# Optimization experiments

Measured on AMD Instinct MI355X. Metric: run time of the kernel, lower is better.

Reference implementation:

```python
import jax, jax.numpy as jnp
import numpy as np

# Mamba2 dims (from source: d_model=2048, d_state=64, d_conv=4, expand=2; defaults headdim=64, ngroups=1)
D_MODEL = 2048
D_STATE = 64
D_CONV = 4
EXPAND = 2
HEADDIM = 64
D_INNER = EXPAND * D_MODEL            # 4096
NHEADS = D_INNER // HEADDIM           # 64
NGROUPS = 1
CONV_DIM = D_INNER + 2 * NGROUPS * D_STATE   # 4224
D_IN_PROJ = 2 * D_INNER + 2 * NGROUPS * D_STATE + NHEADS  # 8384
N_CLASSES = 4
EPS = 1e-5


def setup_inputs() -> dict:
    key = jax.random.key(0)
    ks = jax.random.split(key, 10)
    b, l = 4, 2048
    x = jax.random.normal(ks[0], (b, l, D_MODEL), dtype=jnp.float32)
    in_proj_w = jax.random.normal(ks[1], (D_IN_PROJ, D_MODEL), dtype=jnp.float32) * 0.02
    conv_w = jax.random.normal(ks[2], (CONV_DIM, D_CONV), dtype=jnp.float32) * 0.2
    conv_b = jnp.zeros((CONV_DIM,), dtype=jnp.float32)
    # dt_bias s.t. softplus(dt_bias) in [0.001, 0.1]
    dt = jax.random.uniform(ks[3], (NHEADS,), minval=0.001, maxval=0.1)
    dt_bias = jnp.log(jnp.expm1(dt)).astype(jnp.float32)
    # A in [1, 16] per head
    A_log = jnp.log(jax.random.uniform(ks[4], (NHEADS,), minval=1.0, maxval=16.0)).astype(jnp.float32)
    D = jnp.ones((NHEADS,), dtype=jnp.float32)
    norm_w = jnp.ones((D_INNER,), dtype=jnp.float32)
    out_proj_w = jax.random.normal(ks[5], (D_MODEL, D_INNER), dtype=jnp.float32) * 0.02
    cls_w = jax.random.normal(ks[6], (N_CLASSES, D_MODEL), dtype=jnp.float32) * 0.02
    cls_b = jnp.zeros((N_CLASSES,), dtype=jnp.float32)
    return {"x": x, "in_proj_w": in_proj_w, "conv_w": conv_w, "conv_b": conv_b,
            "dt_bias": dt_bias, "A_log": A_log, "D": D, "norm_w": norm_w,
            "out_proj_w": out_proj_w, "cls_w": cls_w, "cls_b": cls_b}


def _mamba2_forward(x, in_proj_w, conv_w, conv_b, dt_bias, A_log, D, norm_w, out_proj_w):
    b, l, _ = x.shape
    zxbcdt = jnp.einsum('bld,ed->ble', x, in_proj_w)  # (b,l,8384)
    z = zxbcdt[..., :D_INNER]
    xBC = zxbcdt[..., D_INNER:D_INNER + CONV_DIM]
    dt_raw = zxbcdt[..., D_INNER + CONV_DIM:]         # (b,l,nheads)

    # causal depthwise conv1d (kernel D_CONV), then SiLU
    xp = jnp.pad(xBC, ((0, 0), (D_CONV - 1, 0), (0, 0)))
    conv_out = conv_b
    for k in range(D_CONV):
        conv_out = conv_out + xp[:, k:k + l, :] * conv_w[:, k]
    xBC = jax.nn.silu(conv_out)

    xh = xBC[..., :D_INNER].reshape(b, l, NHEADS, HEADDIM)
    Bm = xBC[..., D_INNER:D_INNER + D_STATE]          # (b,l,n) ngroups=1
    Cm = xBC[..., D_INNER + D_STATE:]                 # (b,l,n)

    dt = jax.nn.softplus(dt_raw + dt_bias)           # (b,l,h)
    dA = jnp.exp(dt * (-jnp.exp(A_log)))             # (b,l,h)
    dtx = dt[..., None] * xh                          # (b,l,h,p)

    xs = (dA.transpose(1, 0, 2), dtx.transpose(1, 0, 2, 3),
          Bm.transpose(1, 0, 2), Cm.transpose(1, 0, 2))

    def step(hst, inp):
        dA_t, dtx_t, B_t, C_t = inp
        # hst: (b,h,p,n)
        hst = hst * dA_t[:, :, None, None] + dtx_t[..., None] * B_t[:, None, None, :]
        y_t = jnp.einsum('bhpn,bn->bhp', hst, C_t)
        return hst, y_t

    h0 = jnp.zeros((b, NHEADS, HEADDIM, D_STATE), dtype=x.dtype)
    _, ys = jax.lax.scan(step, h0, xs)               # (l,b,h,p)
    y = ys.transpose(1, 0, 2, 3) + D[None, None, :, None] * xh
    y = y.reshape(b, l, D_INNER)

    # RMSNormGated (norm_before_gate=False): rmsnorm(y * silu(z)) * weight
    y = y * jax.nn.silu(z)
    y = y * jax.lax.rsqrt(jnp.mean(y * y, axis=-1, keepdims=True) + EPS) * norm_w
    return jnp.einsum('ble,de->bld', y, out_proj_w)   # (b,l,d_model)


def reference(x, in_proj_w, conv_w, conv_b, dt_bias, A_log, D, norm_w, out_proj_w, cls_w, cls_b):
    h = _mamba2_forward(x, in_proj_w, conv_w, conv_b, dt_bias, A_log, D, norm_w, out_proj_w)
    return jnp.einsum('bld,cd->blc', h, cls_w) + cls_b  # (b,l,4)
```

## Files before the change

### kernel.cpp

```cpp
#include <hip/hip_runtime.h>

#define BB 4
#define LL 2048
#define DMODEL 2048
#define DSTATE 64
#define DCONV 4
#define DINNER 4096
#define NHEADS 64
#define CONVDIM 4224
#define DINPROJ 8384
#define NPAD1   8448
#define MROWS 8192
#define DTROW0 8320
#define XBCCOLS 4288

typedef short bf16x8 __attribute__((ext_vector_type(8)));
typedef short bf16x4 __attribute__((ext_vector_type(4)));
typedef float f32x4  __attribute__((ext_vector_type(4)));
typedef __attribute__((address_space(1))) void as1_void;
typedef __attribute__((address_space(3))) void as3_void;

__device__ inline unsigned short f2bf(float f) {
  unsigned int u = __float_as_uint(f);
  u += 0x7FFF + ((u >> 16) & 1);
  return (unsigned short)(u >> 16);
}
__device__ inline float bf2f(unsigned short u) {
  return __uint_as_float(((unsigned int)u) << 16);
}

__global__ void f32_to_bf16_kernel(const float* __restrict__ in,
                                   unsigned short* __restrict__ out, long nquads) {
  long q = (long)blockIdx.x * 256 + threadIdx.x;
  if (q >= nquads) return;
  float4 v = ((const float4*)in)[q];
  ushort4 o;
  o.x = f2bf(v.x); o.y = f2bf(v.y); o.z = f2bf(v.z); o.w = f2bf(v.w);
  ((ushort4*)out)[q] = o;
}

__global__ void convert_w1_kernel(const float* __restrict__ w,
                                  unsigned short* __restrict__ out) {
  long q = (long)blockIdx.x * 256 + threadIdx.x;
  long row = q >> 9;
  ushort4 o; o.x = 0; o.y = 0; o.z = 0; o.w = 0;
  if (row < DINPROJ) {
    float4 v = ((const float4*)w)[q];
    o.x = f2bf(v.x); o.y = f2bf(v.y); o.z = f2bf(v.z); o.w = f2bf(v.w);
  }
  ((ushort4*)out)[q] = o;
}

template <bool BF16OUT, bool SPLIT>
__global__ __launch_bounds__(256) void gemm_mfma(
    const unsigned short* __restrict__ A,
    const unsigned short* __restrict__ B,
    void* __restrict__ Cv, void* __restrict__ Cv2,
    int M, int N, int K, int Nsplit, int ld2) {
  __shared__ __align__(16) char sA[128 * 128];
  __shared__ __align__(16) char sB[128 * 128];
  const int tid  = threadIdx.x;
  const int lane = tid & 63;
  const int wave = tid >> 6;
  const int nwg = gridDim.x * gridDim.y;
  int lin = blockIdx.y * gridDim.x + blockIdx.x;
  if ((nwg & 7) == 0) {
    const int q = nwg >> 3;
    lin = (lin & 7) * q + (lin >> 3);
  }
  const long m0 = (long)(lin / gridDim.x) * 128;
  const long n0 = (long)(lin % gridDim.x) * 128;
  const int wm = (wave >> 1) * 64;
  const int wn = (wave & 1) * 64;
  const int fr = lane & 15;
  const int kb = lane >> 4;
  const int xr = (fr & 7) << 4;
  const size_t strideA = (size_t)K * 2;

  f32x4 acc[4][4] = {};

  for (int k0 = 0; k0 < K; k0 += 64) {
    __syncthreads();
#pragma unroll
    for (int u = 0; u < 4; ++u) {
      const int idx  = u * 256 + tid;
      const int row  = idx >> 3;
      const int csrc = ((idx & 7) << 4) ^ ((row & 7) << 4);
      const char* ga = (const char*)A + (size_t)(m0 + row) * strideA + (size_t)k0 * 2 + csrc;
      const char* gb = (const char*)B + (size_t)(n0 + row) * strideA + (size_t)k0 * 2 + csrc;
      __builtin_amdgcn_global_load_lds((as1_void*)ga, (as3_void*)(sA + idx * 16), 16, 0, 0);
      __builtin_amdgcn_global_load_lds((as1_void*)gb, (as3_void*)(sB + idx * 16), 16, 0, 0);
    }
    __syncthreads();
#pragma unroll
    for (int kh = 0; kh < 2; ++kh) {
      bf16x8 af[4], bg[4];
      const int cread = (kh * 64 + kb * 16) ^ xr;
#pragma unroll
      for (int i = 0; i < 4; ++i) {
        const int ar = wm + i * 16 + fr;
        af[i] = *(const bf16x8*)(sA + ar * 128 + cread);
        const int br = wn + i * 16 + fr;
        bg[i] = *(const bf16x8*)(sB + br * 128 + cread);
      }
#pragma unroll
      for (int i = 0; i < 4; ++i)
#pragma unroll
        for (int j = 0; j < 4; ++j)
          acc[i][j] = __builtin_amdgcn_mfma_f32_16x16x32_bf16(af[i], bg[j], acc[i][j], 0, 0, 0);
    }
  }

#pragma unroll
  for (int i = 0; i < 4; ++i) {
    const long mbase = m0 + wm + i * 16 + kb * 4;
#pragma unroll
    for (int j = 0; j < 4; ++j) {
      const long n = n0 + wn + j * 16 + fr;
      if (n < N) {
#pragma unroll
        for (int r = 0; r < 4; ++r) {
          const long m = mbase + r;
          if (!SPLIT || n < Nsplit) {
            const long ld = SPLIT ? Nsplit : N;
            if (BF16OUT) ((unsigned short*)Cv)[m * ld + n] = f2bf(acc[i][j][r]);
            else         ((float*)Cv)[m * ld + n] = acc[i][j][r];
          } else {
            if (BF16OUT) ((unsigned short*)Cv2)[m * (long)ld2 + (n - Nsplit)] = f2bf(acc[i][j][r]);
            else         ((float*)Cv2)[m * (long)ld2 + (n - Nsplit)] = acc[i][j][r];
          }
        }
      }
    }
  }
}

__global__ void dt_kernel(const float* __restrict__ x,
                          const float* __restrict__ w,
                          const float* __restrict__ dt_bias,
                          const float* __restrict__ A_log,
                          float* __restrict__ dtv, float* __restrict__ dAv) {
  __shared__ float s_w[64][129];
  __shared__ float s_x[16][129];
  const int tid = threadIdx.x;
  const int row0 = blockIdx.x * 16;
  const int c = tid & 63;
  const int rg = tid >> 6;
  float acc[4] = {0.f, 0.f, 0.f, 0.f};
  for (int k0 = 0; k0 < DMODEL; k0 += 128) {
    __syncthreads();
#pragma unroll
    for (int u = 0; u < 32; ++u) {
      int idx = u * 256 + tid;
      int r = idx >> 7, kk = idx & 127;
      s_w[r][kk] = w[(size_t)(DTROW0 + r) * DMODEL + k0 + kk];
    }
#pragma unroll
    for (int u = 0; u < 8; ++u) {
      int idx = u * 256 + tid;
      int r = idx >> 7, kk = idx & 127;
      s_x[r][kk] = x[(size_t)(row0 + r) * DMODEL + k0 + kk];
    }
    __syncthreads();
    for (int kk = 0; kk < 128; ++kk) {
      float wv = s_w[c][kk];
#pragma unroll
      for (int j = 0; j < 4; ++j) acc[j] += s_x[rg * 4 + j][kk] * wv;
    }
  }
  const float a = expf(A_log[c]);
  const float bias = dt_bias[c];
#pragma unroll
  for (int j = 0; j < 4; ++j) {
    int row = row0 + rg * 4 + j;
    float v = acc[j] + bias;
    float dt = (v > 20.f) ? v : log1pf(expf(v));
    dtv[(size_t)row * 64 + c] = dt;
    dAv[(size_t)row * 64 + c] = expf(-dt * a);
  }
}

__global__ void conv_kernel(const unsigned short* __restrict__ xbc,
                            const float* __restrict__ conv_w,
                            const float* __restrict__ conv_b,
                            unsigned short* __restrict__ xh,
                            float* __restrict__ Bm,
                            float* __restrict__ Cm) {
  const int row = blockIdx.x;
  const int l = row & (LL - 1);
  const int tid = threadIdx.x;
  for (int gsel = 0; gsel < 3; ++gsel) {
    int g;
    if (gsel == 0) g = tid;
    else if (gsel == 1) g = tid + 256;
    else { if (tid >= 16) break; g = 512 + tid; }
    const int c0 = g * 8;
    float cwa[8][4];
#pragma unroll
    for (int i = 0; i < 8; ++i) {
      float4 cw = *(const float4*)&conv_w[(c0 + i) * 4];
      cwa[i][0] = cw.x; cwa[i][1] = cw.y; cwa[i][2] = cw.z; cwa[i][3] = cw.w;
    }
    float acc[8];
    {
      float4 cb0 = *(const float4*)&conv_b[c0];
      float4 cb1 = *(const float4*)&conv_b[c0 + 4];
      acc[0] = cb0.x; acc[1] = cb0.y; acc[2] = cb0.z; acc[3] = cb0.w;
      acc[4] = cb1.x; acc[5] = cb1.y; acc[6] = cb1.z; acc[7] = cb1.w;
    }
#pragma unroll
    for (int k = 0; k < DCONV; ++k) {
      const int ll = l - (DCONV - 1) + k;
      if (ll >= 0) {
        const size_t rr = (size_t)(row - (DCONV - 1) + k);
        bf16x8 v = *(const bf16x8*)&xbc[rr * XBCCOLS + c0];
#pragma unroll
        for (int i = 0; i < 8; ++i)
          acc[i] += bf2f((unsigned short)v[i]) * cwa[i][k];
      }
    }
    float s[8];
#pragma unroll
    for (int i = 0; i < 8; ++i) s[i] = acc[i] / (1.f + expf(-acc[i]));
    if (g < 512) {
      bf16x8 o;
#pragma unroll
      for (int i = 0; i < 8; ++i) o[i] = (short)f2bf(s[i]);
      *(bf16x8*)&xh[(size_t)row * DINNER + c0] = o;
    } else {
      float4 o0, o1;
      o0.x = s[0]; o0.y = s[1]; o0.z = s[2]; o0.w = s[3];
      o1.x = s[4]; o1.y = s[5]; o1.z = s[6]; o1.w = s[7];
      if (g < 520) {
        float* p = &Bm[(size_t)row * DSTATE + (c0 - DINNER)];
        ((float4*)p)[0] = o0; ((float4*)p)[1] = o1;
      } else {
        float* p = &Cm[(size_t)row * DSTATE + (c0 - DINNER - DSTATE)];
        ((float4*)p)[0] = o0; ((float4*)p)[1] = o1;
      }
    }
  }
}

#define CT 16
#define CHUNK 128
#define NCHUNK 16

__global__ void scan_state_kernel(const unsigned short* __restrict__ xhp,
                                  const float* __restrict__ Bm,
                                  const float* __restrict__ dtv,
                                  const float* __restrict__ dAv,
                                  float* __restrict__ hend,
                                  float* __restrict__ chunkA) {
  __shared__ __align__(16) float s_x[CT][64];
  __shared__ __align__(16) float s_B[CT][64];
  __shared__ float s_dt[CT], s_dA[CT];
  const int chunk = blockIdx.x & (NCHUNK - 1);
  const int bh = blockIdx.x >> 4;
  const int head = bh & 63;
  const int b = bh >> 6;
  const int tid = threadIdx.x;
  const int p = tid >> 2, q = tid & 3, n0 = q * 16;
  const int stt = tid >> 4, scc = (tid & 15) * 4;
  float h[16];
#pragma unroll
  for (int i = 0; i < 16; ++i) h[i] = 0.f;
  float pA = 1.f;
  const int tbase = b * LL + chunk * CHUNK;

  for (int t0 = 0; t0 < CHUNK; t0 += CT) {
    __syncthreads();
    {
      size_t r = (size_t)(tbase + t0 + stt);
      bf16x4 xv = *(const bf16x4*)&xhp[r * DINNER + head * 64 + scc];
      float4 xf;
      xf.x = bf2f((unsigned short)xv[0]); xf.y = bf2f((unsigned short)xv[1]);
      xf.z = bf2f((unsigned short)xv[2]); xf.w = bf2f((unsigned short)xv[3]);
      *(float4*)&s_x[stt][scc] = xf;
      *(float4*)&s_B[stt][scc] = *(const float4*)&Bm[r * 64 + scc];
    }
    if (tid < CT) {
      size_t r = (size_t)(tbase + t0 + tid);
      s_dt[tid] = dtv[r * 64 + head];
      s_dA[tid] = dAv[r * 64 + head];
    }
    __syncthreads();
    for (int tt = 0; tt < CT; ++tt) {
      float dA = s_dA[tt];
      float dtx = s_dt[tt] * s_x[tt][p];
      pA *= dA;
      const float4* Bp = (const float4*)&s_B[tt][n0];
#pragma unroll
      for (int i = 0; i < 4; ++i) {
        float4 bv = Bp[i];
        h[4*i+0] = h[4*i+0] * dA + dtx * bv.x;
        h[4*i+1] = h[4*i+1] * dA + dtx * bv.y;
        h[4*i+2] = h[4*i+2] * dA + dtx * bv.z;
        h[4*i+3] = h[4*i+3] * dA + dtx * bv.w;
      }
    }
  }
  float* hp = hend + ((size_t)bh * NCHUNK + chunk) * 4096 + tid * 16;
#pragma unroll
  for (int i = 0; i < 4; ++i) {
    float4 v; v.x = h[4*i]; v.y = h[4*i+1]; v.z = h[4*i+2]; v.w = h[4*i+3];
    ((float4*)hp)[i] = v;
  }
  if (tid == 0) chunkA[bh * NCHUNK + chunk] = pA;
}

__global__ void scan_prop_kernel(float* __restrict__ hend,
                                 const float* __restrict__ chunkA) {
  const int bh = blockIdx.x;
  const int tid = threadIdx.x;
  float cr[16];
#pragma unroll
  for (int i = 0; i < 16; ++i) cr[i] = 0.f;
  for (int c = 0; c < NCHUNK; ++c) {
    float* hp = hend + ((size_t)bh * NCHUNK + c) * 4096 + tid * 16;
    const float a = chunkA[bh * NCHUNK + c];
    float e[16];
#pragma unroll
    for (int i = 0; i < 4; ++i) {
      float4 v = ((float4*)hp)[i];
      e[4*i] = v.x; e[4*i+1] = v.y; e[4*i+2] = v.z; e[4*i+3] = v.w;
    }
#pragma unroll
    for (int i = 0; i < 4; ++i) {
      float4 v; v.x = cr[4*i]; v.y = cr[4*i+1]; v.z = cr[4*i+2]; v.w = cr[4*i+3];
      ((float4*)hp)[i] = v;
    }
#pragma unroll
    for (int i = 0; i < 16; ++i) cr[i] = cr[i] * a + e[i];
  }
}

__global__ void scan_apply_kernel(const unsigned short* xhp,
                                  const float* __restrict__ Bm,
                                  const float* __restrict__ Cm,
                                  const float* __restrict__ dtv,
                                  const float* __restrict__ dAv,
                                  const float* __restrict__ Dv,
                                  const float* __restrict__ hstart,
                                  unsigned short* y) {
  __shared__ __align__(16) float s_x[CT][64];
  __shared__ __align__(16) float s_B[CT][64];
  __shared__ __align__(16) float s_C[CT][64];
  __shared__ __align__(16) float s_y[CT][64];
  __shared__ float s_dt[CT], s_dA[CT];
  const int chunk = blockIdx.x & (NCHUNK - 1);
  const int bh = blockIdx.x >> 4;
  const int head = bh & 63;
  const int b = bh >> 6;
  const int tid = threadIdx.x;
  const int p = tid >> 2, q = tid & 3, n0 = q * 16;
  const int stt = tid >> 4, scc = (tid & 15) * 4;
  const float Dh = Dv[head];
  const int tbase = b * LL + chunk * CHUNK;

  float h[16];
  {
    const float* hp = hstart + ((size_t)bh * NCHUNK + chunk) * 4096 + tid * 16;
#pragma unroll
    for (int i = 0; i < 4; ++i) {
      float4 v = ((const float4*)hp)[i];
      h[4*i] = v.x; h[4*i+1] = v.y; h[4*i+2] = v.z; h[4*i+3] = v.w;
    }
  }

  for (int t0 = 0; t0 < CHUNK; t0 += CT) {
    __syncthreads();
    {
      size_t r = (size_t)(tbase + t0 + stt);
      bf16x4 xv = *(const bf16x4*)&xhp[r * DINNER + head * 64 + scc];
      float4 xf;
      xf.x = bf2f((unsigned short)xv[0]); xf.y = bf2f((unsigned short)xv[1]);
      xf.z = bf2f((unsigned short)xv[2]); xf.w = bf2f((unsigned short)xv[3]);
      *(float4*)&s_x[stt][scc] = xf;
      *(float4*)&s_B[stt][scc] = *(const float4*)&Bm[r * 64 + scc];
      *(float4*)&s_C[stt][scc] = *(const float4*)&Cm[r * 64 + scc];
    }
    if (tid < CT) {
      size_t r = (size_t)(tbase + t0 + tid);
      s_dt[tid] = dtv[r * 64 + head];
      s_dA[tid] = dAv[r * 64 + head];
    }
    __syncthreads();
    for (int tt = 0; tt < CT; ++tt) {
      float dA = s_dA[tt], dt = s_dt[tt];
      float xp = s_x[tt][p];
      float dtx = dt * xp;
      const float4* Bp = (const float4*)&s_B[tt][n0];
      const float4* Cp = (const float4*)&s_C[tt][n0];
      float ys = 0.f;
#pragma unroll
      for (int i = 0; i < 4; ++i) {
        float4 bv = Bp[i];
        float4 cv = Cp[i];
        h[4*i+0] = h[4*i+0] * dA + dtx * bv.x;  ys += h[4*i+0] * cv.x;
        h[4*i+1] = h[4*i+1] * dA + dtx * bv.y;  ys += h[4*i+1] * cv.y;
        h[4*i+2] = h[4*i+2] * dA + dtx * bv.z;  ys += h[4*i+2] * cv.z;
        h[4*i+3] = h[4*i+3] * dA + dtx * bv.w;  ys += h[4*i+3] * cv.w;
      }
      ys += __shfl_xor(ys, 1);
      ys += __shfl_xor(ys, 2);
      if (q == 0) s_y[tt][p] = ys + Dh * xp;
    }
    __syncthreads();
    {
      size_t r = (size_t)(tbase + t0 + stt);
      float4 yv = *(const float4*)&s_y[stt][scc];
      bf16x4 o;
      o[0] = (short)f2bf(yv.x); o[1] = (short)f2bf(yv.y);
      o[2] = (short)f2bf(yv.z); o[3] = (short)f2bf(yv.w);
      *(bf16x4*)&y[r * DINNER + head * 64 + scc] = o;
    }
  }
}

__global__ void wc_kernel(const float* __restrict__ W,
                          const float* __restrict__ C,
                          float* __restrict__ Wc) {
  const int e = blockIdx.x * 256 + threadIdx.x;
  float a0 = 0, a1 = 0, a2 = 0, a3 = 0;
  for (int d = 0; d < DMODEL; ++d) {
    float wv = W[(size_t)d * DINNER + e];
    a0 += C[d] * wv;
    a1 += C[DMODEL + d] * wv;
    a2 += C[2 * DMODEL + d] * wv;
    a3 += C[3 * DMODEL + d] * wv;
  }
  Wc[e] = a0; Wc[DINNER + e] = a1; Wc[2 * DINNER + e] = a2; Wc[3 * DINNER + e] = a3;
}

__global__ void normcls_kernel(const unsigned short* __restrict__ y,
                               const unsigned short* __restrict__ z,
                               const float* __restrict__ norm_w,
                               const float* __restrict__ Wc,
                               const float* __restrict__ cls_b,
                               float* __restrict__ out) {
  const int row = blockIdx.x;
  const int tid = threadIdx.x;
  const int d0 = tid * 16;
  const size_t base = (size_t)row * DINNER + d0;
  bf16x8 yv0 = *(const bf16x8*)&y[base];
  bf16x8 yv1 = *(const bf16x8*)&y[base + 8];
  bf16x8 zv0 = *(const bf16x8*)&z[base];
  bf16x8 zv1 = *(const bf16x8*)&z[base + 8];
  float g[16];
  float ss = 0.f;
#pragma unroll
  for (int i = 0; i < 8; ++i) {
    float zz = bf2f((unsigned short)zv0[i]);
    float gv = bf2f((unsigned short)yv0[i]) * (zz / (1.f + expf(-zz)));
    g[i] = gv; ss += gv * gv;
  }
#pragma unroll
  for (int i = 0; i < 8; ++i) {
    float zz = bf2f((unsigned short)zv1[i]);
    float gv = bf2f((unsigned short)yv1[i]) * (zz / (1.f + expf(-zz)));
    g[8 + i] = gv; ss += gv * gv;
  }
#pragma unroll
  for (int off = 32; off >= 1; off >>= 1) ss += __shfl_xor(ss, off);
  __shared__ float sred[4];
  __shared__ float s_rs;
  if ((tid & 63) == 0) sred[tid >> 6] = ss;
  __syncthreads();
  if (tid == 0)
    s_rs = rsqrtf((sred[0] + sred[1] + sred[2] + sred[3]) / (float)DINNER + 1e-5f);
  __syncthreads();
  const float rs = s_rs;
  float gn[16];
#pragma unroll
  for (int j = 0; j < 4; ++j) {
    float4 nw = *(const float4*)&norm_w[d0 + j * 4];
    gn[j*4+0] = g[j*4+0] * rs * nw.x;
    gn[j*4+1] = g[j*4+1] * rs * nw.y;
    gn[j*4+2] = g[j*4+2] * rs * nw.z;
    gn[j*4+3] = g[j*4+3] * rs * nw.w;
  }
  float a[4] = {0.f, 0.f, 0.f, 0.f};
#pragma unroll
  for (int c = 0; c < 4; ++c) {
#pragma unroll
    for (int j = 0; j < 4; ++j) {
      float4 w4 = *(const float4*)&Wc[c * DINNER + d0 + j * 4];
      a[c] += gn[j*4+0]*w4.x + gn[j*4+1]*w4.y + gn[j*4+2]*w4.z + gn[j*4+3]*w4.w;
    }
  }
#pragma unroll
  for (int off = 32; off >= 1; off >>= 1) {
#pragma unroll
    for (int c = 0; c < 4; ++c) a[c] += __shfl_xor(a[c], off);
  }
  __shared__ float s4[4][4];
  if ((tid & 63) == 0) {
    int w = tid >> 6;
    s4[w][0] = a[0]; s4[w][1] = a[1]; s4[w][2] = a[2]; s4[w][3] = a[3];
  }
  __syncthreads();
  if (tid < 4)
    out[(size_t)row * 4 + tid] = s4[0][tid] + s4[1][tid] + s4[2][tid] + s4[3][tid] + cls_b[tid];
}

extern "C" void kernel_launch(void* const* d_in, const int* in_sizes, int n_in,
                              void* d_out, int out_size, void* d_ws, size_t ws_size,
                              hipStream_t stream) {
  const float* x          = (const float*)d_in[0];
  const float* in_proj_w  = (const float*)d_in[1];
  const float* conv_w     = (const float*)d_in[2];
  const float* conv_b     = (const float*)d_in[3];
  const float* dt_bias    = (const float*)d_in[4];
  const float* A_log      = (const float*)d_in[5];
  const float* Dv         = (const float*)d_in[6];
  const float* norm_w     = (const float*)d_in[7];
  const float* out_proj_w = (const float*)d_in[8];
  const float* cls_w      = (const float*)d_in[9];
  const float* cls_b      = (const float*)d_in[10];

  char* ws = (char*)d_ws;
  unsigned short* zbuf = (unsigned short*)(ws + 0);
  unsigned short* xbc  = (unsigned short*)(ws + 67108864);
  unsigned short* xh   = (unsigned short*)(ws + 137363456);
  float*          Bmp  = (float*)(ws + 204472320);
  float*          Cmp  = (float*)(ws + 206569472);
  float*          dtv  = (float*)(ws + 208666624);
  float*          dAv  = (float*)(ws + 210763776);
  unsigned short* xbf = xh;
  unsigned short* w1b = (unsigned short*)((char*)xh + 33554432);
  float*          hend   = (float*)xbc;
  float*          chunkA = (float*)(ws + 134217728);
  float*          Wcp    = (float*)(ws + 134234112);

  f32_to_bf16_kernel<<<16384, 256, 0, stream>>>(x, xbf, 4194304);
  convert_w1_kernel<<<16896, 256, 0, stream>>>(in_proj_w, w1b);

  dt_kernel<<<512, 256, 0, stream>>>(x, in_proj_w, dt_bias, A_log, dtv, dAv);

  gemm_mfma<true, true><<<dim3(NPAD1 / 128, MROWS / 128), 256, 0, stream>>>(
      xbf, w1b, zbuf, xbc, MROWS, DINPROJ, DMODEL, DINNER, XBCCOLS);

  conv_kernel<<<MROWS, 256, 0, stream>>>(xbc, conv_w, conv_b, xh, Bmp, Cmp);

  wc_kernel<<<16, 256, 0, stream>>>(out_proj_w, cls_w, Wcp);

  scan_state_kernel<<<256 * NCHUNK, 256, 0, stream>>>(xh, Bmp, dtv, dAv, hend, chunkA);
  scan_prop_kernel<<<256, 256, 0, stream>>>(hend, chunkA);
  scan_apply_kernel<<<256 * NCHUNK, 256, 0, stream>>>(xh, Bmp, Cmp, dtv, dAv, Dv, hend, xh);

  normcls_kernel<<<MROWS, 256, 0, stream>>>(xh, zbuf, norm_w, Wcp, cls_b, (float*)d_out);
}
```

Baseline: 1.548 ms.

## Use 256x256 double-buffered GEMM, fuse x bf16 cast into dt, split wc reduction

The in_proj GEMM moves to 256x256 tiles with 512 threads and double-buffered async global-to-LDS loads, so the next K tile loads while the current one is computed. The standalone f32-to-bf16 conversion of x is folded into dt_kernel, which already reads x. The serial wc_kernel, which ran only 16 blocks, is split into a 16x16-block partial-sum kernel plus a reduce kernel for more parallelism. The 128KB LDS per block limits occupancy, and NPAD1/256 = 33 columns gives a grid of 33x32 tiles.

```diff
diff --git a/kernel.cpp b/kernel.cpp
--- a/kernel.cpp
+++ b/kernel.cpp
@@ -29,16 +29,6 @@
   return __uint_as_float(((unsigned int)u) << 16);
 }
 
-__global__ void f32_to_bf16_kernel(const float* __restrict__ in,
-                                   unsigned short* __restrict__ out, long nquads) {
-  long q = (long)blockIdx.x * 256 + threadIdx.x;
-  if (q >= nquads) return;
-  float4 v = ((const float4*)in)[q];
-  ushort4 o;
-  o.x = f2bf(v.x); o.y = f2bf(v.y); o.z = f2bf(v.z); o.w = f2bf(v.w);
-  ((ushort4*)out)[q] = o;
-}
-
 __global__ void convert_w1_kernel(const float* __restrict__ w,
                                   unsigned short* __restrict__ out) {
   long q = (long)blockIdx.x * 256 + threadIdx.x;
@@ -52,82 +42,96 @@
 }
 
 template <bool BF16OUT, bool SPLIT>
-__global__ __launch_bounds__(256) void gemm_mfma(
+__global__ __launch_bounds__(512, 2) void gemm_mfma256(
     const unsigned short* __restrict__ A,
     const unsigned short* __restrict__ B,
     void* __restrict__ Cv, void* __restrict__ Cv2,
     int M, int N, int K, int Nsplit, int ld2) {
-  __shared__ __align__(16) char sA[128 * 128];
-  __shared__ __align__(16) char sB[128 * 128];
+  __shared__ __align__(16) char lds[131072];
   const int tid  = threadIdx.x;
   const int lane = tid & 63;
   const int wave = tid >> 6;
   const int nwg = gridDim.x * gridDim.y;
   int lin = blockIdx.y * gridDim.x + blockIdx.x;
-  if ((nwg & 7) == 0) {
-    const int q = nwg >> 3;
-    lin = (lin & 7) * q + (lin >> 3);
-  }
-  const long m0 = (long)(lin / gridDim.x) * 128;
-  const long n0 = (long)(lin % gridDim.x) * 128;
-  const int wm = (wave >> 1) * 64;
-  const int wn = (wave & 1) * 64;
+  if ((nwg & 7) == 0) { const int q = nwg >> 3; lin = (lin & 7) * q + (lin >> 3); }
+  const long m0 = (long)(lin / gridDim.x) * 256;
+  const long n0 = (long)(lin % gridDim.x) * 256;
+  const int wm = wave >> 2;
+  const int wn = wave & 3;
   const int fr = lane & 15;
   const int kb = lane >> 4;
   const int xr = (fr & 7) << 4;
-  const size_t strideA = (size_t)K * 2;
-
-  f32x4 acc[4][4] = {};
-
-  for (int k0 = 0; k0 < K; k0 += 64) {
-    __syncthreads();
-#pragma unroll
-    for (int u = 0; u < 4; ++u) {
-      const int idx  = u * 256 + tid;
-      const int row  = idx >> 3;
-      const int csrc = ((idx & 7) << 4) ^ ((row & 7) << 4);
-      const char* ga = (const char*)A + (size_t)(m0 + row) * strideA + (size_t)k0 * 2 + csrc;
-      const char* gb = (const char*)B + (size_t)(n0 + row) * strideA + (size_t)k0 * 2 + csrc;
-      __builtin_amdgcn_global_load_lds((as1_void*)ga, (as3_void*)(sA + idx * 16), 16, 0, 0);
-      __builtin_amdgcn_global_load_lds((as1_void*)gb, (as3_void*)(sB + idx * 16), 16, 0, 0);
-    }
-    __syncthreads();
-#pragma unroll
-    for (int kh = 0; kh < 2; ++kh) {
-      bf16x8 af[4], bg[4];
-      const int cread = (kh * 64 + kb * 16) ^ xr;
-#pragma unroll
-      for (int i = 0; i < 4; ++i) {
-        const int ar = wm + i * 16 + fr;
-        af[i] = *(const bf16x8*)(sA + ar * 128 + cread);
-        const int br = wn + i * 16 + fr;
-        bg[i] = *(const bf16x8*)(sB + br * 128 + cread);
+  const size_t sb = (size_t)K * 2;
+
+  f32x4 acc[8][4] = {};
+
+  const int NT = K / 64;
+
+  auto stage = [&](int kt, int b) {
+#pragma unroll
+    for (int u = 0; u < 8; ++u) {
+      const int idx  = u * 512 + tid;
+      const int half = idx >> 11;
+      const int r    = (idx & 2047) >> 3;
+      const int csrc = ((idx & 7) << 4) ^ ((r & 7) << 4);
+      const char* g = half
+          ? (const char*)B + (size_t)(n0 + r) * sb + (size_t)kt * 128 + csrc
+          : (const char*)A + (size_t)(m0 + r) * sb + (size_t)kt * 128 + csrc;
+      __builtin_amdgcn_global_load_lds((as1_void*)g,
+          (as3_void*)(lds + b * 65536 + half * 32768 + (idx & 2047) * 16), 16, 0, 0);
+    }
+  };
+
+  stage(0, 0);
+  stage(1, 1);
+
+  for (int kt = 0; kt < NT; ++kt) {
+    const int b = kt & 1;
+    if (kt + 1 < NT) asm volatile("s_waitcnt vmcnt(8)" ::: "memory");
+    else             asm volatile("s_waitcnt vmcnt(0)" ::: "memory");
+    __builtin_amdgcn_s_barrier();
+    __builtin_amdgcn_sched_barrier(0);
+    const char* la = lds + b * 65536;
+    const char* lb = la + 32768;
+#pragma unroll
+    for (int ks = 0; ks < 2; ++ks) {
+      const int cread = (ks * 64 + kb * 16) ^ xr;
+      bf16x8 bg[4];
+#pragma unroll
+      for (int nf = 0; nf < 4; ++nf)
+        bg[nf] = *(const bf16x8*)(lb + (wn * 64 + nf * 16 + fr) * 128 + cread);
+#pragma unroll
+      for (int mf = 0; mf < 8; ++mf) {
+        bf16x8 af = *(const bf16x8*)(la + (wm * 128 + mf * 16 + fr) * 128 + cread);
+#pragma unroll
+        for (int nf = 0; nf < 4; ++nf)
+          acc[mf][nf] = __builtin_amdgcn_mfma_f32_16x16x32_bf16(af, bg[nf], acc[mf][nf], 0, 0, 0);
       }
-#pragma unroll
-      for (int i = 0; i < 4; ++i)
-#pragma unroll
-        for (int j = 0; j < 4; ++j)
-          acc[i][j] = __builtin_amdgcn_mfma_f32_16x16x32_bf16(af[i], bg[j], acc[i][j], 0, 0, 0);
-    }
-  }
-
-#pragma unroll
-  for (int i = 0; i < 4; ++i) {
-    const long mbase = m0 + wm + i * 16 + kb * 4;
-#pragma unroll
-    for (int j = 0; j < 4; ++j) {
-      const long n = n0 + wn + j * 16 + fr;
+    }
+    __builtin_amdgcn_sched_barrier(0);
+    asm volatile("" ::: "memory");
+    __builtin_amdgcn_s_barrier();
+    __builtin_amdgcn_sched_barrier(0);
+    if (kt + 2 < NT) stage(kt + 2, b);
+  }
+
+#pragma unroll
+  for (int mf = 0; mf < 8; ++mf) {
+    const long mbase = m0 + wm * 128 + mf * 16 + kb * 4;
+#pragma unroll
+    for (int nf = 0; nf < 4; ++nf) {
+      const long n = n0 + wn * 64 + nf * 16 + fr;
       if (n < N) {
 #pragma unroll
         for (int r = 0; r < 4; ++r) {
           const long m = mbase + r;
           if (!SPLIT || n < Nsplit) {
             const long ld = SPLIT ? Nsplit : N;
-            if (BF16OUT) ((unsigned short*)Cv)[m * ld + n] = f2bf(acc[i][j][r]);
-            else         ((float*)Cv)[m * ld + n] = acc[i][j][r];
+            if (BF16OUT) ((unsigned short*)Cv)[m * ld + n] = f2bf(acc[mf][nf][r]);
+            else         ((float*)Cv)[m * ld + n] = acc[mf][nf][r];
           } else {
-            if (BF16OUT) ((unsigned short*)Cv2)[m * (long)ld2 + (n - Nsplit)] = f2bf(acc[i][j][r]);
-            else         ((float*)Cv2)[m * (long)ld2 + (n - Nsplit)] = acc[i][j][r];
+            if (BF16OUT) ((unsigned short*)Cv2)[m * (long)ld2 + (n - Nsplit)] = f2bf(acc[mf][nf][r]);
+            else         ((float*)Cv2)[m * (long)ld2 + (n - Nsplit)] = acc[mf][nf][r];
           }
         }
       }
@@ -139,7 +143,8 @@
                           const float* __restrict__ w,
                           const float* __restrict__ dt_bias,
                           const float* __restrict__ A_log,
-                          float* __restrict__ dtv, float* __restrict__ dAv) {
+                          float* __restrict__ dtv, float* __restrict__ dAv,
+                          unsigned short* __restrict__ xbf) {
   __shared__ float s_w[64][129];
   __shared__ float s_x[16][129];
   const int tid = threadIdx.x;
@@ -159,7 +164,9 @@
     for (int u = 0; u < 8; ++u) {
       int idx = u * 256 + tid;
       int r = idx >> 7, kk = idx & 127;
-      s_x[r][kk] = x[(size_t)(row0 + r) * DMODEL + k0 + kk];
+      float v = x[(size_t)(row0 + r) * DMODEL + k0 + kk];
+      s_x[r][kk] = v;
+      xbf[(size_t)(row0 + r) * DMODEL + k0 + kk] = f2bf(v);
     }
     __syncthreads();
     for (int kk = 0; kk < 128; ++kk) {
@@ -418,19 +425,29 @@
   }
 }
 
-__global__ void wc_kernel(const float* __restrict__ W,
-                          const float* __restrict__ C,
-                          float* __restrict__ Wc) {
+__global__ void wc_part_kernel(const float* __restrict__ W,
+                               const float* __restrict__ C,
+                               float* __restrict__ part) {
   const int e = blockIdx.x * 256 + threadIdx.x;
+  const int d0 = blockIdx.y * 128;
   float a0 = 0, a1 = 0, a2 = 0, a3 = 0;
-  for (int d = 0; d < DMODEL; ++d) {
+  for (int d = d0; d < d0 + 128; ++d) {
     float wv = W[(size_t)d * DINNER + e];
     a0 += C[d] * wv;
     a1 += C[DMODEL + d] * wv;
     a2 += C[2 * DMODEL + d] * wv;
     a3 += C[3 * DMODEL + d] * wv;
   }
-  Wc[e] = a0; Wc[DINNER + e] = a1; Wc[2 * DINNER + e] = a2; Wc[3 * DINNER + e] = a3;
+  float* pp = part + (size_t)blockIdx.y * 4 * DINNER;
+  pp[e] = a0; pp[DINNER + e] = a1; pp[2 * DINNER + e] = a2; pp[3 * DINNER + e] = a3;
+}
+__global__ void wc_reduce_kernel(const float* __restrict__ part,
+                                 float* __restrict__ Wc) {
+  const int i = blockIdx.x * 256 + threadIdx.x;
+  float s = 0.f;
+#pragma unroll
+  for (int p = 0; p < 16; ++p) s += part[(size_t)p * 4 * DINNER + i];
+  Wc[i] = s;
 }
 
 __global__ void normcls_kernel(const unsigned short* __restrict__ y,
@@ -532,18 +549,19 @@
   float*          hend   = (float*)xbc;
   float*          chunkA = (float*)(ws + 134217728);
   float*          Wcp    = (float*)(ws + 134234112);
-
-  f32_to_bf16_kernel<<<16384, 256, 0, stream>>>(x, xbf, 4194304);
+  float*          wcpart = (float*)(ws + 134299648);
+
+  dt_kernel<<<512, 256, 0, stream>>>(x, in_proj_w, dt_bias, A_log, dtv, dAv, xbf);
+
   convert_w1_kernel<<<16896, 256, 0, stream>>>(in_proj_w, w1b);
 
-  dt_kernel<<<512, 256, 0, stream>>>(x, in_proj_w, dt_bias, A_log, dtv, dAv);
-
-  gemm_mfma<true, true><<<dim3(NPAD1 / 128, MROWS / 128), 256, 0, stream>>>(
+  gemm_mfma256<true, true><<<dim3(NPAD1 / 256, MROWS / 256), 512, 0, stream>>>(
       xbf, w1b, zbuf, xbc, MROWS, DINPROJ, DMODEL, DINNER, XBCCOLS);
 
   conv_kernel<<<MROWS, 256, 0, stream>>>(xbc, conv_w, conv_b, xh, Bmp, Cmp);
 
-  wc_kernel<<<16, 256, 0, stream>>>(out_proj_w, cls_w, Wcp);
+  wc_part_kernel<<<dim3(16, 16), 256, 0, stream>>>(out_proj_w, cls_w, wcpart);
+  wc_reduce_kernel<<<64, 256, 0, stream>>>(wcpart, Wcp);
 
   scan_state_kernel<<<256 * NCHUNK, 256, 0, stream>>>(xh, Bmp, dtv, dAv, hend, chunkA);
   scan_prop_kernel<<<256, 256, 0, stream>>>(hend, chunkA);
```

Measured after the change: 1.348 ms. 12.9% less time.
